# Kernel tuning notes

Hardware: AMD Instinct MI355X
Metric: run time of the kernel (lower is better)

## Reference

```python
import jax, jax.numpy as jnp
import numpy as np

N_HEAD = 16

def setup_inputs() -> dict:
    key = jax.random.key(0)
    k1, k2, k3 = jax.random.split(key, 3)
    C = 1024
    x = jax.random.normal(k1, (2, 2048, C), dtype=jnp.float32)
    W_attn = jax.random.normal(k2, (C, 3 * C), dtype=jnp.float32) * (C ** -0.5)
    b_attn = jnp.zeros((3 * C,), dtype=jnp.float32)
    W_proj = jax.random.normal(k3, (C, C), dtype=jnp.float32) * (C ** -0.5)
    b_proj = jnp.zeros((C,), dtype=jnp.float32)
    return {"x": x, "W_attn": W_attn, "b_attn": b_attn, "W_proj": W_proj, "b_proj": b_proj}

def reference(x, W_attn, b_attn, W_proj, b_proj):
    B, T, C = x.shape
    H = N_HEAD
    hd = C // H
    qkv = x @ W_attn + b_attn                      # [B,T,3C]
    q, k, v = jnp.split(qkv, 3, axis=-1)
    q = q.reshape(B, T, H, hd).transpose(0, 2, 1, 3)  # [B,H,T,hd]
    k = k.reshape(B, T, H, hd).transpose(0, 2, 1, 3)
    v = v.reshape(B, T, H, hd).transpose(0, 2, 1, 3)
    att = jnp.einsum('bhqd,bhkd->bhqk', q, k) * (1.0 / jnp.sqrt(jnp.float32(hd)))
    causal = jnp.tril(jnp.ones((T, T), dtype=bool))
    att = jnp.where(causal[None, None, :, :], att, jnp.float32(-jnp.inf))
    att = jax.nn.softmax(att, axis=-1)
    y = jnp.einsum('bhqk,bhkd->bhqd', att, v)       # [B,H,T,hd]
    y = y.transpose(0, 2, 1, 3).reshape(B, T, C)
    return y @ W_proj + b_proj
```

## Files before the change

kernel.cpp:

```cpp
#include <hip/hip_runtime.h>
#include <hip/hip_bf16.h>

typedef unsigned short u16;
using frag_ab = __attribute__((ext_vector_type(8))) short;
using f32x4   = __attribute__((ext_vector_type(4))) float;
using u16x4   = __attribute__((ext_vector_type(4))) unsigned short;
using u16x8   = __attribute__((ext_vector_type(8))) unsigned short;

#define N_CTX   2048
#define NBATCH  2
#define CDIM    1024
#define NH      16
#define HD      64

__device__ __forceinline__ u16 f2b(float f) {
  __hip_bfloat16 h = __float2bfloat16(f);
  return __builtin_bit_cast(u16, h);
}

__device__ __forceinline__ f32x4 mfma16(frag_ab a, frag_ab b, f32x4 c) {
  return __builtin_amdgcn_mfma_f32_16x16x32_bf16(a, b, c, 0, 0, 0);
}

#define GLDS16(src, dst) \
  __builtin_amdgcn_global_load_lds((const __attribute__((address_space(1))) void*)(src), \
                                   (__attribute__((address_space(3))) void*)(dst), 16, 0, 0)

__global__ __launch_bounds__(256) void prep_all(const float* __restrict__ x, u16* __restrict__ xb,
                                                const float* __restrict__ Wa, u16* __restrict__ Wab,
                                                const float* __restrict__ Wp, u16* __restrict__ Wpb) {
  __shared__ float tile[32][33];
  const int blk = blockIdx.x;
  if (blk < 2048) {
    int i = blk * 256 + threadIdx.x;
    const f32x4* ip = (const f32x4*)x;
    f32x4 a = ip[2 * i], b2 = ip[2 * i + 1];
    u16x8 r;
    #pragma unroll
    for (int j = 0; j < 4; ++j) { r[j] = f2b(a[j]); r[4 + j] = f2b(b2[j]); }
    ((u16x8*)xb)[i] = r;
    return;
  }
  const float* in; u16* out; int K, N, bx, by;
  if (blk < 5120) {
    int idx = blk - 2048; in = Wa; out = Wab; K = CDIM; N = 3 * CDIM;
    bx = idx % 96; by = idx / 96;
  } else {
    int idx = blk - 5120; in = Wp; out = Wpb; K = CDIM; N = CDIM;
    bx = idx & 31; by = idx >> 5;
  }
  int n0 = bx * 32, k0 = by * 32;
  int c = threadIdx.x & 31, r0 = threadIdx.x >> 5;
  #pragma unroll
  for (int i = 0; i < 4; ++i) {
    int r = r0 + i * 8;
    tile[r][c] = in[(size_t)(k0 + r) * N + n0 + c];
  }
  __syncthreads();
  #pragma unroll
  for (int i = 0; i < 4; ++i) {
    int r = r0 + i * 8;
    out[(size_t)(n0 + r) * K + k0 + c] = f2b(tile[c][r]);
  }
}

__global__ __launch_bounds__(512, 4) void gemm_qkv128(const u16* __restrict__ A,
                                                      const u16* __restrict__ Bt,
                                                      const float* __restrict__ bias,
                                                      u16* __restrict__ Qo, u16* __restrict__ Ko,
                                                      u16* __restrict__ Vto) {
  __shared__ __align__(16) u16 As[2][128 * 64];
  __shared__ __align__(16) u16 Bs[2][192 * 64];
  const int tid = threadIdx.x, w = tid >> 6, lane = tid & 63;
  const int g = lane >> 4, lr = lane & 15;
  const int wr = w >> 2, wc = w & 3;
  const int bid = blockIdx.x;
  const int swz = (bid & 7) * 64 + (bid >> 3);
  const int tm = (swz & 31) * 128, tn = (swz >> 5) * 192;

  f32x4 acc[4][3];
  #pragma unroll
  for (int mi = 0; mi < 4; ++mi)
    #pragma unroll
    for (int ni = 0; ni < 3; ++ni)
      acc[mi][ni] = (f32x4){0.f, 0.f, 0.f, 0.f};

  auto STAGE = [&](int d, int kt) {
    const int k0 = kt << 6;
    #pragma unroll
    for (int j = 0; j < 2; ++j) {
      int ci = j * 512 + tid, row = ci >> 3, c8 = ci & 7;
      GLDS16(A + (size_t)(tm + row) * CDIM + k0 + ((c8 ^ (row & 7)) << 3),
             &As[d][row * 64 + c8 * 8]);
    }
    #pragma unroll
    for (int j = 0; j < 3; ++j) {
      int ci = j * 512 + tid, row = ci >> 3, c8 = ci & 7;
      GLDS16(Bt + (size_t)(tn + row) * CDIM + k0 + ((c8 ^ (row & 7)) << 3),
             &Bs[d][row * 64 + c8 * 8]);
    }
  };

  STAGE(0, 0);
  asm volatile("s_waitcnt vmcnt(0)" ::: "memory");
  __builtin_amdgcn_s_barrier();

  const int x7 = lr & 7;
  for (int t = 0; t < 16; ++t) {
    const int cur = t & 1;
    if (t < 15) STAGE(cur ^ 1, t + 1);

    frag_ab af[4][2], bf[3][2];
    #pragma unroll
    for (int mi = 0; mi < 4; ++mi) {
      int row = wr * 64 + mi * 16 + lr;
      #pragma unroll
      for (int ks = 0; ks < 2; ++ks)
        af[mi][ks] = *(const frag_ab*)&As[cur][row * 64 + ((((ks << 2) | g) ^ x7) << 3)];
    }
    #pragma unroll
    for (int ni = 0; ni < 3; ++ni) {
      int row = wc * 48 + ni * 16 + lr;
      #pragma unroll
      for (int ks = 0; ks < 2; ++ks)
        bf[ni][ks] = *(const frag_ab*)&Bs[cur][row * 64 + ((((ks << 2) | g) ^ x7) << 3)];
    }
    __builtin_amdgcn_s_setprio(1);
    #pragma unroll
    for (int mi = 0; mi < 4; ++mi)
      #pragma unroll
      for (int ni = 0; ni < 3; ++ni)
        #pragma unroll
        for (int ks = 0; ks < 2; ++ks)
          acc[mi][ni] = mfma16(af[mi][ks], bf[ni][ks], acc[mi][ni]);
    __builtin_amdgcn_s_setprio(0);

    asm volatile("s_waitcnt vmcnt(0)" ::: "memory");
    __builtin_amdgcn_s_barrier();
  }

  #pragma unroll
  for (int ni = 0; ni < 3; ++ni) {
    int n = tn + wc * 48 + ni * 16 + lr;
    float bv = bias[n];
    int which = n >> 10, c = n & 1023, h = c >> 6, d = c & 63;
    #pragma unroll
    for (int mi = 0; mi < 4; ++mi) {
      if (which == 2) {
        int t0 = tm + wr * 64 + mi * 16 + g * 4;
        int bb = t0 >> 11, tt = t0 & (N_CTX - 1);
        u16x4 pk;
        #pragma unroll
        for (int r = 0; r < 4; ++r) pk[r] = f2b(acc[mi][ni][r] + bv);
        *(u16x4*)&Vto[((size_t)(bb * NH + h) * HD + d) * N_CTX + tt] = pk;
      } else {
        u16* dst = (which == 0) ? Qo : Ko;
        float scl = (which == 0) ? 0.180336881f : 1.0f;
        #pragma unroll
        for (int r = 0; r < 4; ++r) {
          int m = tm + wr * 64 + mi * 16 + g * 4 + r;
          int bb = m >> 11, tt = m & (N_CTX - 1);
          dst[((size_t)(bb * NH + h) * N_CTX + tt) * HD + d] = f2b((acc[mi][ni][r] + bv) * scl);
        }
      }
    }
  }
}

__global__ __launch_bounds__(512, 4) void gemm_proj128(const u16* __restrict__ A,
                                                       const u16* __restrict__ Bt,
                                                       const float* __restrict__ bias,
                                                       float* __restrict__ out) {
  __shared__ __align__(16) u16 As[2][128 * 64];
  __shared__ __align__(16) u16 Bs[2][64 * 64];
  const int tid = threadIdx.x, w = tid >> 6, lane = tid & 63;
  const int g = lane >> 4, lr = lane & 15;
  const int wr = w >> 1, wc = w & 1;
  const int bid = blockIdx.x;
  const int swz = (bid & 7) * 64 + (bid >> 3);
  const int tm = (swz & 31) * 128, tn = (swz >> 5) * 64;

  f32x4 acc[2][2];
  #pragma unroll
  for (int mi = 0; mi < 2; ++mi)
    #pragma unroll
    for (int ni = 0; ni < 2; ++ni)
      acc[mi][ni] = (f32x4){0.f, 0.f, 0.f, 0.f};

  auto STAGE = [&](int d, int kt) {
    const int k0 = kt << 6;
    #pragma unroll
    for (int j = 0; j < 2; ++j) {
      int ci = j * 512 + tid, row = ci >> 3, c8 = ci & 7;
      GLDS16(A + (size_t)(tm + row) * CDIM + k0 + ((c8 ^ (row & 7)) << 3),
             &As[d][row * 64 + c8 * 8]);
    }
    {
      int row = tid >> 3, c8 = tid & 7;
      GLDS16(Bt + (size_t)(tn + row) * CDIM + k0 + ((c8 ^ (row & 7)) << 3),
             &Bs[d][row * 64 + c8 * 8]);
    }
  };

  STAGE(0, 0);
  asm volatile("s_waitcnt vmcnt(0)" ::: "memory");
  __builtin_amdgcn_s_barrier();

  const int x7 = lr & 7;
  for (int t = 0; t < 16; ++t) {
    const int cur = t & 1;
    if (t < 15) STAGE(cur ^ 1, t + 1);

    frag_ab af[2][2], bf[2][2];
    #pragma unroll
    for (int mi = 0; mi < 2; ++mi) {
      int row = wr * 32 + mi * 16 + lr;
      #pragma unroll
      for (int ks = 0; ks < 2; ++ks)
        af[mi][ks] = *(const frag_ab*)&As[cur][row * 64 + ((((ks << 2) | g) ^ x7) << 3)];
    }
    #pragma unroll
    for (int ni = 0; ni < 2; ++ni) {
      int row = wc * 32 + ni * 16 + lr;
      #pragma unroll
      for (int ks = 0; ks < 2; ++ks)
        bf[ni][ks] = *(const frag_ab*)&Bs[cur][row * 64 + ((((ks << 2) | g) ^ x7) << 3)];
    }
    __builtin_amdgcn_s_setprio(1);
    #pragma unroll
    for (int mi = 0; mi < 2; ++mi)
      #pragma unroll
      for (int ni = 0; ni < 2; ++ni)
        #pragma unroll
        for (int ks = 0; ks < 2; ++ks)
          acc[mi][ni] = mfma16(af[mi][ks], bf[ni][ks], acc[mi][ni]);
    __builtin_amdgcn_s_setprio(0);

    asm volatile("s_waitcnt vmcnt(0)" ::: "memory");
    __builtin_amdgcn_s_barrier();
  }

  #pragma unroll
  for (int ni = 0; ni < 2; ++ni) {
    int n = tn + wc * 32 + ni * 16 + lr;
    float bv = bias[n];
    #pragma unroll
    for (int mi = 0; mi < 2; ++mi)
      #pragma unroll
      for (int r = 0; r < 4; ++r) {
        int m = tm + wr * 32 + mi * 16 + g * 4 + r;
        out[(size_t)m * CDIM + n] = acc[mi][ni][r] + bv;
      }
  }
}

__global__ __launch_bounds__(512, 4) void attn_fwd(const u16* __restrict__ Q, const u16* __restrict__ K,
                                                   const u16* __restrict__ Vt, u16* __restrict__ Y) {
  __shared__ __align__(16) u16 Ks[4][64 * 64];
  __shared__ __align__(16) u16 Vs[4][64 * 64];
  const int orig = blockIdx.x;
  const int swz = (orig & 7) * 64 + (orig >> 3);
  const int bh = swz >> 4;
  const int p  = swz & 15;
  const int qtb = 31 - p;
  const int tid = threadIdx.x, w = tid >> 6, lane = tid & 63;
  const int grp = w >> 2, wq = w & 3;
  const int qt  = grp ? qtb : p;
  const int g = lane >> 4, lr = lane & 15;
  const size_t base = (size_t)bh * N_CTX * HD;
  const u16* Kbh = K + base;
  const u16* Vbh = Vt + base;

  const int c8 = tid & 7, srow = tid >> 3;
  const size_t kOff = (size_t)srow * HD + (size_t)((c8 ^ (srow & 7)) * 8);
  const size_t vOff = (size_t)srow * N_CTX + (size_t)((c8 ^ (srow & 7)) * 8);

  frag_ab qf[2];
  {
    const u16* qp = Q + base + (size_t)(qt * 64 + wq * 16 + lr) * HD + g * 8;
    qf[0] = *(const frag_ab*)qp;  qf[1] = *(const frag_ab*)(qp + 32);
  }

  float ps = 0.f;
  f32x4 o[4];
  #pragma unroll
  for (int d = 0; d < 4; ++d) o[d] = (f32x4){0.f, 0.f, 0.f, 0.f};

  auto STAGE = [&](int b, int kt) {
    GLDS16(Kbh + (size_t)kt * 64 * HD + kOff, &Ks[b][(size_t)tid * 8]);
    GLDS16(Vbh + (size_t)kt * 64 + vOff,      &Vs[b][(size_t)tid * 8]);
  };

  const int npair = (qtb + 2) >> 1;
  STAGE(0, 0);
  STAGE(1, 1);
  asm volatile("s_waitcnt vmcnt(0)" ::: "memory");
  __builtin_amdgcn_s_barrier();

  for (int i = 0; i < npair; ++i) {
    const int t0 = 2 * i, t1 = 2 * i + 1;
    const int b0 = t0 & 3, b1 = t1 & 3;
    if (i + 1 < npair) { STAGE((t0 + 2) & 3, t0 + 2); STAGE((t1 + 2) & 3, t1 + 2); }

    if (t0 <= qt) {
      frag_ab kf[8][2];
      #pragma unroll
      for (int nf = 0; nf < 4; ++nf)
        #pragma unroll
        for (int ks = 0; ks < 2; ++ks) {
          kf[nf][ks]     = *(const frag_ab*)&Ks[b0][(size_t)(nf * 16 + lr) * 64 +
                                                    (size_t)((((ks << 2) | g) ^ (lr & 7)) * 8)];
          kf[4 + nf][ks] = *(const frag_ab*)&Ks[b1][(size_t)(nf * 16 + lr) * 64 +
                                                    (size_t)((((ks << 2) | g) ^ (lr & 7)) * 8)];
        }
      f32x4 s[8];
      __builtin_amdgcn_s_setprio(1);
      #pragma unroll
      for (int j = 0; j < 8; ++j) {
        f32x4 a = (f32x4){0.f, 0.f, 0.f, 0.f};
        a = mfma16(kf[j][0], qf[0], a);
        a = mfma16(kf[j][1], qf[1], a);
        s[j] = a;
      }
      __builtin_amdgcn_s_setprio(0);
      const int qrow = wq * 16 + lr;
      if (t0 == qt) {
        #pragma unroll
        for (int nf = 0; nf < 4; ++nf)
          #pragma unroll
          for (int r = 0; r < 4; ++r)
            if (nf * 16 + g * 4 + r > qrow) s[nf][r] = -1e30f;
      }
      if (t1 >= qt) {
        const int off = (t1 - qt) * 64;
        #pragma unroll
        for (int nf = 0; nf < 4; ++nf)
          #pragma unroll
          for (int r = 0; r < 4; ++r)
            if (off + nf * 16 + g * 4 + r > qrow) s[4 + nf][r] = -1e30f;
      }
      #pragma unroll
      for (int j = 0; j < 8; ++j)
        #pragma unroll
        for (int r = 0; r < 4; ++r)
          s[j][r] = __builtin_amdgcn_exp2f(s[j][r]);
      float ts[8];
      #pragma unroll
      for (int j = 0; j < 8; ++j)
        ts[j] = (s[j][0] + s[j][1]) + (s[j][2] + s[j][3]);
      ps += ((ts[0] + ts[1]) + (ts[2] + ts[3])) + ((ts[4] + ts[5]) + (ts[6] + ts[7]));
      frag_ab pa[4];
      #pragma unroll
      for (int ks = 0; ks < 4; ++ks)
        #pragma unroll
        for (int j = 0; j < 4; ++j) {
          pa[ks][j]     = (short)f2b(s[2 * ks][j]);
          pa[ks][4 + j] = (short)f2b(s[2 * ks + 1][j]);
        }
      #pragma unroll
      for (int d = 0; d < 4; ++d) {
        const int row = (d * 16 + lr) * 64;
        frag_ab vf[4];
        #pragma unroll
        for (int ks = 0; ks < 2; ++ks) {
          u16x4 lo0 = *(const u16x4*)&Vs[b0][row + (((ks * 4 + (g >> 1)) ^ (lr & 7)) * 8) + (g & 1) * 4];
          u16x4 hi0 = *(const u16x4*)&Vs[b0][row + (((ks * 4 + 2 + (g >> 1)) ^ (lr & 7)) * 8) + (g & 1) * 4];
          u16x4 lo1 = *(const u16x4*)&Vs[b1][row + (((ks * 4 + (g >> 1)) ^ (lr & 7)) * 8) + (g & 1) * 4];
          u16x4 hi1 = *(const u16x4*)&Vs[b1][row + (((ks * 4 + 2 + (g >> 1)) ^ (lr & 7)) * 8) + (g & 1) * 4];
          #pragma unroll
          for (int j = 0; j < 4; ++j) {
            vf[ks][j] = (short)lo0[j];      vf[ks][4 + j] = (short)hi0[j];
            vf[2 + ks][j] = (short)lo1[j];  vf[2 + ks][4 + j] = (short)hi1[j];
          }
        }
        __builtin_amdgcn_s_setprio(1);
        #pragma unroll
        for (int ks = 0; ks < 4; ++ks)
          o[d] = mfma16(pa[ks], vf[ks], o[d]);
        __builtin_amdgcn_s_setprio(0);
      }
    }

    asm volatile("s_waitcnt vmcnt(0)" ::: "memory");
    __builtin_amdgcn_s_barrier();
  }

  const int b = bh >> 4, h = bh & 15;
  float sum = ps;
  sum += __shfl_xor(sum, 16, 64);
  sum += __shfl_xor(sum, 32, 64);
  float li = 1.0f / sum;
  #pragma unroll
  for (int r = 0; r < 4; ++r) {
    int src = (lane & 48) | (((lane >> 4) & 3) * 4 + r);
    float lir = __shfl(li, src, 64);
    int row = qt * 64 + wq * 16 + g * 4 + r;
    #pragma unroll
    for (int d = 0; d < 4; ++d)
      Y[((size_t)(b * N_CTX + row)) * CDIM + h * HD + d * 16 + lr] = f2b(o[d][r] * lir);
  }
}

extern "C" void kernel_launch(void* const* d_in, const int* in_sizes, int n_in,
                              void* d_out, int out_size, void* d_ws, size_t ws_size,
                              hipStream_t stream) {
  const float* x      = (const float*)d_in[0];
  const float* W_attn = (const float*)d_in[1];
  const float* b_attn = (const float*)d_in[2];
  const float* W_proj = (const float*)d_in[3];
  const float* b_proj = (const float*)d_in[4];
  float* out = (float*)d_out;
  char* ws = (char*)d_ws;

  u16* xb  = (u16*)(ws);
  u16* Wab = (u16*)(ws + ((size_t)8 << 20));
  u16* Wpb = (u16*)(ws + ((size_t)14 << 20));
  u16* Qb  = (u16*)(ws + ((size_t)16 << 20));
  u16* Kb  = (u16*)(ws + ((size_t)24 << 20));
  u16* Vtb = (u16*)(ws + ((size_t)32 << 20));
  u16* yb  = xb;

  prep_all<<<6144, 256, 0, stream>>>(x, xb, W_attn, Wab, W_proj, Wpb);
  gemm_qkv128<<<512, 512, 0, stream>>>(xb, Wab, b_attn, Qb, Kb, Vtb);
  attn_fwd<<<512, 512, 0, stream>>>(Qb, Kb, Vtb, yb);
  gemm_proj128<<<512, 512, 0, stream>>>(yb, Wpb, b_proj, out);
}
```

Measured before the change: 91.75 us.

## Split KV tiles across wave groups, each computing both query tiles, merge via LDS

Before, the two wave groups each handled one query tile (short and long) over all KV tiles, so the short-tile group sat idle for most of the loop. Now each group takes alternate KV tiles and computes partial outputs for both query tiles, skipping the short tile once past its diagonal. The partial outputs and row sums are merged through shared memory at the end. This balances work between the groups, at the cost of more accumulator registers and an extra LDS reduction step.

```diff
diff --git a/kernel.cpp b/kernel.cpp
--- a/kernel.cpp
+++ b/kernel.cpp
@@ -262,10 +262,9 @@
   const int swz = (orig & 7) * 64 + (orig >> 3);
   const int bh = swz >> 4;
   const int p  = swz & 15;
-  const int qtb = 31 - p;
+  const int qta = p, qtb = 31 - p;
   const int tid = threadIdx.x, w = tid >> 6, lane = tid & 63;
   const int grp = w >> 2, wq = w & 3;
-  const int qt  = grp ? qtb : p;
   const int g = lane >> 4, lr = lane & 15;
   const size_t base = (size_t)bh * N_CTX * HD;
   const u16* Kbh = K + base;
@@ -275,16 +274,18 @@
   const size_t kOff = (size_t)srow * HD + (size_t)((c8 ^ (srow & 7)) * 8);
   const size_t vOff = (size_t)srow * N_CTX + (size_t)((c8 ^ (srow & 7)) * 8);
 
-  frag_ab qf[2];
+  frag_ab qfA[2], qfB[2];
   {
-    const u16* qp = Q + base + (size_t)(qt * 64 + wq * 16 + lr) * HD + g * 8;
-    qf[0] = *(const frag_ab*)qp;  qf[1] = *(const frag_ab*)(qp + 32);
-  }
-
-  float ps = 0.f;
-  f32x4 o[4];
-  #pragma unroll
-  for (int d = 0; d < 4; ++d) o[d] = (f32x4){0.f, 0.f, 0.f, 0.f};
+    const u16* qa = Q + base + (size_t)(qta * 64 + wq * 16 + lr) * HD + g * 8;
+    qfA[0] = *(const frag_ab*)qa;  qfA[1] = *(const frag_ab*)(qa + 32);
+    const u16* qb = Q + base + (size_t)(qtb * 64 + wq * 16 + lr) * HD + g * 8;
+    qfB[0] = *(const frag_ab*)qb;  qfB[1] = *(const frag_ab*)(qb + 32);
+  }
+
+  float psA = 0.f, psB = 0.f;
+  f32x4 oA[4], oB[4];
+  #pragma unroll
+  for (int d = 0; d < 4; ++d) { oA[d] = (f32x4){0,0,0,0}; oB[d] = (f32x4){0,0,0,0}; }
 
   auto STAGE = [&](int b, int kt) {
     GLDS16(Kbh + (size_t)kt * 64 * HD + kOff, &Ks[b][(size_t)tid * 8]);
@@ -297,86 +298,105 @@
   asm volatile("s_waitcnt vmcnt(0)" ::: "memory");
   __builtin_amdgcn_s_barrier();
 
+  const int qrow = wq * 16 + lr;
   for (int i = 0; i < npair; ++i) {
-    const int t0 = 2 * i, t1 = 2 * i + 1;
-    const int b0 = t0 & 3, b1 = t1 & 3;
-    if (i + 1 < npair) { STAGE((t0 + 2) & 3, t0 + 2); STAGE((t1 + 2) & 3, t1 + 2); }
-
-    if (t0 <= qt) {
-      frag_ab kf[8][2];
+    const int t = 2 * i + grp;
+    const int bb = t & 3;
+    const int t0 = 2 * i;
+    if (i + 1 < npair) { STAGE((t0 + 2) & 3, t0 + 2); STAGE((t0 + 3) & 3, t0 + 3); }
+
+    if (t <= qtb) {
+      frag_ab kf[4][2];
       #pragma unroll
       for (int nf = 0; nf < 4; ++nf)
         #pragma unroll
-        for (int ks = 0; ks < 2; ++ks) {
-          kf[nf][ks]     = *(const frag_ab*)&Ks[b0][(size_t)(nf * 16 + lr) * 64 +
-                                                    (size_t)((((ks << 2) | g) ^ (lr & 7)) * 8)];
-          kf[4 + nf][ks] = *(const frag_ab*)&Ks[b1][(size_t)(nf * 16 + lr) * 64 +
-                                                    (size_t)((((ks << 2) | g) ^ (lr & 7)) * 8)];
+        for (int ks = 0; ks < 2; ++ks)
+          kf[nf][ks] = *(const frag_ab*)&Ks[bb][(size_t)(nf * 16 + lr) * 64 +
+                                               (size_t)((((ks << 2) | g) ^ (lr & 7)) * 8)];
+      const bool actA = (t <= qta);
+      f32x4 sB[4], sA[4];
+      __builtin_amdgcn_s_setprio(1);
+      #pragma unroll
+      for (int j = 0; j < 4; ++j) {
+        f32x4 a = (f32x4){0.f, 0.f, 0.f, 0.f};
+        a = mfma16(kf[j][0], qfB[0], a);
+        a = mfma16(kf[j][1], qfB[1], a);
+        sB[j] = a;
+      }
+      if (actA) {
+        #pragma unroll
+        for (int j = 0; j < 4; ++j) {
+          f32x4 a = (f32x4){0.f, 0.f, 0.f, 0.f};
+          a = mfma16(kf[j][0], qfA[0], a);
+          a = mfma16(kf[j][1], qfA[1], a);
+          sA[j] = a;
         }
-      f32x4 s[8];
-      __builtin_amdgcn_s_setprio(1);
-      #pragma unroll
-      for (int j = 0; j < 8; ++j) {
-        f32x4 a = (f32x4){0.f, 0.f, 0.f, 0.f};
-        a = mfma16(kf[j][0], qf[0], a);
-        a = mfma16(kf[j][1], qf[1], a);
-        s[j] = a;
       }
       __builtin_amdgcn_s_setprio(0);
-      const int qrow = wq * 16 + lr;
-      if (t0 == qt) {
+      if (t == qtb) {
         #pragma unroll
         for (int nf = 0; nf < 4; ++nf)
           #pragma unroll
           for (int r = 0; r < 4; ++r)
-            if (nf * 16 + g * 4 + r > qrow) s[nf][r] = -1e30f;
-      }
-      if (t1 >= qt) {
-        const int off = (t1 - qt) * 64;
+            if (nf * 16 + g * 4 + r > qrow) sB[nf][r] = -1e30f;
+      }
+      if (t == qta) {
         #pragma unroll
         for (int nf = 0; nf < 4; ++nf)
           #pragma unroll
           for (int r = 0; r < 4; ++r)
-            if (off + nf * 16 + g * 4 + r > qrow) s[4 + nf][r] = -1e30f;
-      }
-      #pragma unroll
-      for (int j = 0; j < 8; ++j)
+            if (nf * 16 + g * 4 + r > qrow) sA[nf][r] = -1e30f;
+      }
+      #pragma unroll
+      for (int j = 0; j < 4; ++j)
         #pragma unroll
         for (int r = 0; r < 4; ++r)
-          s[j][r] = __builtin_amdgcn_exp2f(s[j][r]);
-      float ts[8];
-      #pragma unroll
-      for (int j = 0; j < 8; ++j)
-        ts[j] = (s[j][0] + s[j][1]) + (s[j][2] + s[j][3]);
-      ps += ((ts[0] + ts[1]) + (ts[2] + ts[3])) + ((ts[4] + ts[5]) + (ts[6] + ts[7]));
-      frag_ab pa[4];
-      #pragma unroll
-      for (int ks = 0; ks < 4; ++ks)
+          sB[j][r] = __builtin_amdgcn_exp2f(sB[j][r]);
+      psB += ((sB[0][0]+sB[0][1])+(sB[0][2]+sB[0][3])) + ((sB[1][0]+sB[1][1])+(sB[1][2]+sB[1][3]))
+           + ((sB[2][0]+sB[2][1])+(sB[2][2]+sB[2][3])) + ((sB[3][0]+sB[3][1])+(sB[3][2]+sB[3][3]));
+      frag_ab paB[2];
+      #pragma unroll
+      for (int ks = 0; ks < 2; ++ks)
         #pragma unroll
         for (int j = 0; j < 4; ++j) {
-          pa[ks][j]     = (short)f2b(s[2 * ks][j]);
-          pa[ks][4 + j] = (short)f2b(s[2 * ks + 1][j]);
+          paB[ks][j]     = (short)f2b(sB[2 * ks][j]);
+          paB[ks][4 + j] = (short)f2b(sB[2 * ks + 1][j]);
         }
+      frag_ab paA[2];
+      if (actA) {
+        #pragma unroll
+        for (int j = 0; j < 4; ++j)
+          #pragma unroll
+          for (int r = 0; r < 4; ++r)
+            sA[j][r] = __builtin_amdgcn_exp2f(sA[j][r]);
+        psA += ((sA[0][0]+sA[0][1])+(sA[0][2]+sA[0][3])) + ((sA[1][0]+sA[1][1])+(sA[1][2]+sA[1][3]))
+             + ((sA[2][0]+sA[2][1])+(sA[2][2]+sA[2][3])) + ((sA[3][0]+sA[3][1])+(sA[3][2]+sA[3][3]));
+        #pragma unroll
+        for (int ks = 0; ks < 2; ++ks)
+          #pragma unroll
+          for (int j = 0; j < 4; ++j) {
+            paA[ks][j]     = (short)f2b(sA[2 * ks][j]);
+            paA[ks][4 + j] = (short)f2b(sA[2 * ks + 1][j]);
+          }
+      }
       #pragma unroll
       for (int d = 0; d < 4; ++d) {
         const int row = (d * 16 + lr) * 64;
-        frag_ab vf[4];
+        frag_ab vf[2];
         #pragma unroll
         for (int ks = 0; ks < 2; ++ks) {
-          u16x4 lo0 = *(const u16x4*)&Vs[b0][row + (((ks * 4 + (g >> 1)) ^ (lr & 7)) * 8) + (g & 1) * 4];
-          u16x4 hi0 = *(const u16x4*)&Vs[b0][row + (((ks * 4 + 2 + (g >> 1)) ^ (lr & 7)) * 8) + (g & 1) * 4];
-          u16x4 lo1 = *(const u16x4*)&Vs[b1][row + (((ks * 4 + (g >> 1)) ^ (lr & 7)) * 8) + (g & 1) * 4];
-          u16x4 hi1 = *(const u16x4*)&Vs[b1][row + (((ks * 4 + 2 + (g >> 1)) ^ (lr & 7)) * 8) + (g & 1) * 4];
+          u16x4 lo = *(const u16x4*)&Vs[bb][row + (((ks * 4 + (g >> 1)) ^ (lr & 7)) * 8) + (g & 1) * 4];
+          u16x4 hi = *(const u16x4*)&Vs[bb][row + (((ks * 4 + 2 + (g >> 1)) ^ (lr & 7)) * 8) + (g & 1) * 4];
           #pragma unroll
-          for (int j = 0; j < 4; ++j) {
-            vf[ks][j] = (short)lo0[j];      vf[ks][4 + j] = (short)hi0[j];
-            vf[2 + ks][j] = (short)lo1[j];  vf[2 + ks][4 + j] = (short)hi1[j];
-          }
+          for (int j = 0; j < 4; ++j) { vf[ks][j] = (short)lo[j]; vf[ks][4 + j] = (short)hi[j]; }
         }
         __builtin_amdgcn_s_setprio(1);
-        #pragma unroll
-        for (int ks = 0; ks < 4; ++ks)
-          o[d] = mfma16(pa[ks], vf[ks], o[d]);
+        oB[d] = mfma16(paB[0], vf[0], oB[d]);
+        oB[d] = mfma16(paB[1], vf[1], oB[d]);
+        if (actA) {
+          oA[d] = mfma16(paA[0], vf[0], oA[d]);
+          oA[d] = mfma16(paA[1], vf[1], oA[d]);
+        }
         __builtin_amdgcn_s_setprio(0);
       }
     }
@@ -385,19 +405,58 @@
     __builtin_amdgcn_s_barrier();
   }
 
+  psA += __shfl_xor(psA, 16, 64);  psA += __shfl_xor(psA, 32, 64);
+  psB += __shfl_xor(psB, 16, 64);  psB += __shfl_xor(psB, 32, 64);
+
+  float* SA  = (float*)&Ks[0][0];
+  float* SB  = (float*)&Vs[0][0];
+  float* PSA = (float*)&Ks[2][0];
+  float* PSB = PSA + 64;
+
+  if (grp == 1) {
+    #pragma unroll
+    for (int d = 0; d < 4; ++d)
+      #pragma unroll
+      for (int r = 0; r < 4; ++r)
+        SA[(wq * 16 + g * 4 + r) * 64 + d * 16 + lr] = oA[d][r];
+    if (g == 0) PSA[wq * 16 + lr] = psA;
+  } else {
+    #pragma unroll
+    for (int d = 0; d < 4; ++d)
+      #pragma unroll
+      for (int r = 0; r < 4; ++r)
+        SB[(wq * 16 + g * 4 + r) * 64 + d * 16 + lr] = oB[d][r];
+    if (g == 0) PSB[wq * 16 + lr] = psB;
+  }
+  __syncthreads();
+
   const int b = bh >> 4, h = bh & 15;
-  float sum = ps;
-  sum += __shfl_xor(sum, 16, 64);
-  sum += __shfl_xor(sum, 32, 64);
-  float li = 1.0f / sum;
-  #pragma unroll
-  for (int r = 0; r < 4; ++r) {
-    int src = (lane & 48) | (((lane >> 4) & 3) * 4 + r);
-    float lir = __shfl(li, src, 64);
-    int row = qt * 64 + wq * 16 + g * 4 + r;
-    #pragma unroll
-    for (int d = 0; d < 4; ++d)
-      Y[((size_t)(b * N_CTX + row)) * CDIM + h * HD + d * 16 + lr] = f2b(o[d][r] * lir);
+  if (grp == 0) {
+    float li = 1.0f / (psA + PSA[wq * 16 + lr]);
+    #pragma unroll
+    for (int r = 0; r < 4; ++r) {
+      int src = (lane & 48) | (((lane >> 4) & 3) * 4 + r);
+      float lir = __shfl(li, src, 64);
+      int row = qta * 64 + wq * 16 + g * 4 + r;
+      #pragma unroll
+      for (int d = 0; d < 4; ++d) {
+        float val = (oA[d][r] + SA[(wq * 16 + g * 4 + r) * 64 + d * 16 + lr]) * lir;
+        Y[((size_t)(b * N_CTX + row)) * CDIM + h * HD + d * 16 + lr] = f2b(val);
+      }
+    }
+  } else {
+    float li = 1.0f / (psB + PSB[wq * 16 + lr]);
+    #pragma unroll
+    for (int r = 0; r < 4; ++r) {
+      int src = (lane & 48) | (((lane >> 4) & 3) * 4 + r);
+      float lir = __shfl(li, src, 64);
+      int row = qtb * 64 + wq * 16 + g * 4 + r;
+      #pragma unroll
+      for (int d = 0; d < 4; ++d) {
+        float val = (oB[d][r] + SB[(wq * 16 + g * 4 + r) * 64 + d * 16 + lr]) * lir;
+        Y[((size_t)(b * N_CTX + row)) * CDIM + h * HD + d * 16 + lr] = f2b(val);
+      }
+    }
   }
 }
 
```

Measured after the change: 109.1 us. 18.9% more time.

## Split KV range across two wave groups per query tile, merge via LDS

Applied to the files above, without the earlier changes.

Previously each block paired two query tiles (p and 31-p) across its two 4-wave groups to balance causal work. Now each block handles a single query tile, and the two wave groups process alternating KV tiles. Their partial outputs and row sums are combined through shared memory at the end. The grid doubles to 1024 blocks, ordered so the longest tiles are scheduled first. This gives more parallelism per query tile and more blocks, at the cost of a reduction through LDS, an extra barrier, and possible load imbalance between the two groups on the last odd tile.

```diff
diff --git a/kernel.cpp b/kernel.cpp
--- a/kernel.cpp
+++ b/kernel.cpp
@@ -259,13 +259,10 @@
   __shared__ __align__(16) u16 Ks[4][64 * 64];
   __shared__ __align__(16) u16 Vs[4][64 * 64];
   const int orig = blockIdx.x;
-  const int swz = (orig & 7) * 64 + (orig >> 3);
-  const int bh = swz >> 4;
-  const int p  = swz & 15;
-  const int qtb = 31 - p;
+  const int bh = (orig & 7) * 4 + ((orig >> 3) & 3);
+  const int qt = 31 - (orig >> 5);
   const int tid = threadIdx.x, w = tid >> 6, lane = tid & 63;
   const int grp = w >> 2, wq = w & 3;
-  const int qt  = grp ? qtb : p;
   const int g = lane >> 4, lr = lane & 15;
   const size_t base = (size_t)bh * N_CTX * HD;
   const u16* Kbh = K + base;
@@ -291,67 +288,54 @@
     GLDS16(Vbh + (size_t)kt * 64 + vOff,      &Vs[b][(size_t)tid * 8]);
   };
 
-  const int npair = (qtb + 2) >> 1;
+  const int niter = (qt + 2) >> 1;
   STAGE(0, 0);
   STAGE(1, 1);
   asm volatile("s_waitcnt vmcnt(0)" ::: "memory");
   __builtin_amdgcn_s_barrier();
 
-  for (int i = 0; i < npair; ++i) {
-    const int t0 = 2 * i, t1 = 2 * i + 1;
-    const int b0 = t0 & 3, b1 = t1 & 3;
-    if (i + 1 < npair) { STAGE((t0 + 2) & 3, t0 + 2); STAGE((t1 + 2) & 3, t1 + 2); }
-
-    if (t0 <= qt) {
-      frag_ab kf[8][2];
+  const int qrow = wq * 16 + lr;
+  for (int i = 0; i < niter; ++i) {
+    const int t0 = 2 * i;
+    const int t  = t0 + grp;
+    if (i + 1 < niter) { STAGE((t0 + 2) & 3, t0 + 2); STAGE((t0 + 3) & 3, t0 + 3); }
+
+    if (t <= qt) {
+      const int bb = t & 3;
+      frag_ab kf[4][2];
       #pragma unroll
       for (int nf = 0; nf < 4; ++nf)
         #pragma unroll
-        for (int ks = 0; ks < 2; ++ks) {
-          kf[nf][ks]     = *(const frag_ab*)&Ks[b0][(size_t)(nf * 16 + lr) * 64 +
-                                                    (size_t)((((ks << 2) | g) ^ (lr & 7)) * 8)];
-          kf[4 + nf][ks] = *(const frag_ab*)&Ks[b1][(size_t)(nf * 16 + lr) * 64 +
-                                                    (size_t)((((ks << 2) | g) ^ (lr & 7)) * 8)];
-        }
-      f32x4 s[8];
+        for (int ks = 0; ks < 2; ++ks)
+          kf[nf][ks] = *(const frag_ab*)&Ks[bb][(size_t)(nf * 16 + lr) * 64 +
+                                                (size_t)((((ks << 2) | g) ^ (lr & 7)) * 8)];
+      f32x4 s[4];
       __builtin_amdgcn_s_setprio(1);
       #pragma unroll
-      for (int j = 0; j < 8; ++j) {
+      for (int j = 0; j < 4; ++j) {
         f32x4 a = (f32x4){0.f, 0.f, 0.f, 0.f};
         a = mfma16(kf[j][0], qf[0], a);
         a = mfma16(kf[j][1], qf[1], a);
         s[j] = a;
       }
       __builtin_amdgcn_s_setprio(0);
-      const int qrow = wq * 16 + lr;
-      if (t0 == qt) {
+      if (t == qt) {
         #pragma unroll
         for (int nf = 0; nf < 4; ++nf)
           #pragma unroll
           for (int r = 0; r < 4; ++r)
             if (nf * 16 + g * 4 + r > qrow) s[nf][r] = -1e30f;
       }
-      if (t1 >= qt) {
-        const int off = (t1 - qt) * 64;
-        #pragma unroll
-        for (int nf = 0; nf < 4; ++nf)
-          #pragma unroll
-          for (int r = 0; r < 4; ++r)
-            if (off + nf * 16 + g * 4 + r > qrow) s[4 + nf][r] = -1e30f;
-      }
-      #pragma unroll
-      for (int j = 0; j < 8; ++j)
+      #pragma unroll
+      for (int j = 0; j < 4; ++j)
         #pragma unroll
         for (int r = 0; r < 4; ++r)
           s[j][r] = __builtin_amdgcn_exp2f(s[j][r]);
-      float ts[8];
-      #pragma unroll
-      for (int j = 0; j < 8; ++j)
-        ts[j] = (s[j][0] + s[j][1]) + (s[j][2] + s[j][3]);
-      ps += ((ts[0] + ts[1]) + (ts[2] + ts[3])) + ((ts[4] + ts[5]) + (ts[6] + ts[7]));
-      frag_ab pa[4];
-      #pragma unroll
-      for (int ks = 0; ks < 4; ++ks)
+      ps += ((s[0][0]+s[0][1])+(s[0][2]+s[0][3])) + ((s[1][0]+s[1][1])+(s[1][2]+s[1][3]))
+          + ((s[2][0]+s[2][1])+(s[2][2]+s[2][3])) + ((s[3][0]+s[3][1])+(s[3][2]+s[3][3]));
+      frag_ab pa[2];
+      #pragma unroll
+      for (int ks = 0; ks < 2; ++ks)
         #pragma unroll
         for (int j = 0; j < 4; ++j) {
           pa[ks][j]     = (short)f2b(s[2 * ks][j]);
@@ -360,23 +344,17 @@
       #pragma unroll
       for (int d = 0; d < 4; ++d) {
         const int row = (d * 16 + lr) * 64;
-        frag_ab vf[4];
+        frag_ab vf[2];
         #pragma unroll
         for (int ks = 0; ks < 2; ++ks) {
-          u16x4 lo0 = *(const u16x4*)&Vs[b0][row + (((ks * 4 + (g >> 1)) ^ (lr & 7)) * 8) + (g & 1) * 4];
-          u16x4 hi0 = *(const u16x4*)&Vs[b0][row + (((ks * 4 + 2 + (g >> 1)) ^ (lr & 7)) * 8) + (g & 1) * 4];
-          u16x4 lo1 = *(const u16x4*)&Vs[b1][row + (((ks * 4 + (g >> 1)) ^ (lr & 7)) * 8) + (g & 1) * 4];
-          u16x4 hi1 = *(const u16x4*)&Vs[b1][row + (((ks * 4 + 2 + (g >> 1)) ^ (lr & 7)) * 8) + (g & 1) * 4];
+          u16x4 lo = *(const u16x4*)&Vs[bb][row + (((ks * 4 + (g >> 1)) ^ (lr & 7)) * 8) + (g & 1) * 4];
+          u16x4 hi = *(const u16x4*)&Vs[bb][row + (((ks * 4 + 2 + (g >> 1)) ^ (lr & 7)) * 8) + (g & 1) * 4];
           #pragma unroll
-          for (int j = 0; j < 4; ++j) {
-            vf[ks][j] = (short)lo0[j];      vf[ks][4 + j] = (short)hi0[j];
-            vf[2 + ks][j] = (short)lo1[j];  vf[2 + ks][4 + j] = (short)hi1[j];
-          }
+          for (int j = 0; j < 4; ++j) { vf[ks][j] = (short)lo[j]; vf[ks][4 + j] = (short)hi[j]; }
         }
         __builtin_amdgcn_s_setprio(1);
-        #pragma unroll
-        for (int ks = 0; ks < 4; ++ks)
-          o[d] = mfma16(pa[ks], vf[ks], o[d]);
+        o[d] = mfma16(pa[0], vf[0], o[d]);
+        o[d] = mfma16(pa[1], vf[1], o[d]);
         __builtin_amdgcn_s_setprio(0);
       }
     }
@@ -385,19 +363,36 @@
     __builtin_amdgcn_s_barrier();
   }
 
-  const int b = bh >> 4, h = bh & 15;
-  float sum = ps;
-  sum += __shfl_xor(sum, 16, 64);
-  sum += __shfl_xor(sum, 32, 64);
-  float li = 1.0f / sum;
-  #pragma unroll
-  for (int r = 0; r < 4; ++r) {
-    int src = (lane & 48) | (((lane >> 4) & 3) * 4 + r);
-    float lir = __shfl(li, src, 64);
-    int row = qt * 64 + wq * 16 + g * 4 + r;
+  ps += __shfl_xor(ps, 16, 64);
+  ps += __shfl_xor(ps, 32, 64);
+
+  float* SO = (float*)&Ks[0][0];
+  float* PS = (float*)&Vs[0][0];
+
+  if (grp == 1) {
     #pragma unroll
     for (int d = 0; d < 4; ++d)
-      Y[((size_t)(b * N_CTX + row)) * CDIM + h * HD + d * 16 + lr] = f2b(o[d][r] * lir);
+      #pragma unroll
+      for (int r = 0; r < 4; ++r)
+        SO[(wq * 16 + g * 4 + r) * 64 + d * 16 + lr] = o[d][r];
+    if (g == 0) PS[wq * 16 + lr] = ps;
+  }
+  __syncthreads();
+
+  if (grp == 0) {
+    const int b = bh >> 4, h = bh & 15;
+    float li = 1.0f / (ps + PS[wq * 16 + lr]);
+    #pragma unroll
+    for (int r = 0; r < 4; ++r) {
+      int src = (lane & 48) | (((lane >> 4) & 3) * 4 + r);
+      float lir = __shfl(li, src, 64);
+      int row = qt * 64 + wq * 16 + g * 4 + r;
+      #pragma unroll
+      for (int d = 0; d < 4; ++d) {
+        float val = (o[d][r] + SO[(wq * 16 + g * 4 + r) * 64 + d * 16 + lr]) * lir;
+        Y[((size_t)(b * N_CTX + row)) * CDIM + h * HD + d * 16 + lr] = f2b(val);
+      }
+    }
   }
 }
 
@@ -422,6 +417,6 @@
 
   prep_all<<<6144, 256, 0, stream>>>(x, xb, W_attn, Wab, W_proj, Wpb);
   gemm_qkv128<<<512, 512, 0, stream>>>(xb, Wab, b_attn, Qb, Kb, Vtb);
-  attn_fwd<<<512, 512, 0, stream>>>(Qb, Kb, Vtb, yb);
+  attn_fwd<<<1024, 512, 0, stream>>>(Qb, Kb, Vtb, yb);
   gemm_proj128<<<512, 512, 0, stream>>>(yb, Wpb, b_proj, out);
 }
```

After: 89.41 us. 2.6% less time.
